# Kernel tuning notes

Measured on AMD Instinct MI355X. Metric: run time of the kernel, lower is better.

The kernel has to match this reference:

```python
import jax, jax.numpy as jnp
import numpy as np

N_SUPPORT = 131072
NUM_CLASSES = 1024
D = 512
NUM_LEVELS = 3
LN_EPS = 1e-5


def setup_inputs() -> dict:
    key = jax.random.key(0)
    ks = jax.random.split(key, 10)
    s = 1.0 / np.sqrt(D)
    return {
        "support_features": jax.random.normal(ks[0], (N_SUPPORT, D), dtype=jnp.float32),
        "support_labels": jax.random.randint(ks[1], (N_SUPPORT,), 0, NUM_CLASSES, dtype=jnp.int32),
        "W1": jax.random.normal(ks[2], (NUM_LEVELS, D, D), dtype=jnp.float32) * s,
        "b1": jnp.zeros((NUM_LEVELS, D), dtype=jnp.float32),
        "ln_gamma": jnp.ones((NUM_LEVELS, D), dtype=jnp.float32),
        "ln_beta": jnp.zeros((NUM_LEVELS, D), dtype=jnp.float32),
        "W2": jax.random.normal(ks[3], (NUM_LEVELS, D, D), dtype=jnp.float32) * s,
        "b2": jnp.zeros((NUM_LEVELS, D), dtype=jnp.float32),
        "level_temperatures": jnp.ones((NUM_LEVELS,), dtype=jnp.float32),
    }


def _prototype_level(x, labels, w1, bb1, gamma, beta, w2, bb2, counts):
    # MLP: Linear -> LayerNorm -> ReLU -> (Dropout=identity, eval) -> Linear
    h = x @ w1 + bb1                                   # [N, D]
    mu = jnp.mean(h, axis=-1, keepdims=True)
    var = jnp.mean(jnp.square(h - mu), axis=-1, keepdims=True)
    h = (h - mu) * jax.lax.rsqrt(var + LN_EPS) * gamma + beta
    h = jax.nn.relu(h)
    h = h @ w2 + bb2                                   # [N, D]
    # per-class mean prototype (segment mean)
    sums = jax.ops.segment_sum(h, labels, num_segments=NUM_CLASSES)  # [C, D]
    return sums / counts


def reference(support_features, support_labels, W1, b1, ln_gamma, ln_beta, W2, b2, level_temperatures):
    labels = support_labels.astype(jnp.int32)
    counts = jax.ops.segment_sum(
        jnp.ones((support_features.shape[0],), dtype=support_features.dtype),
        labels, num_segments=NUM_CLASSES)
    counts = jnp.maximum(counts, 1.0)[:, None]         # [C, 1]

    level_protos = jax.vmap(
        lambda w1, bb1, g, bt, w2, bb2: _prototype_level(
            support_features, labels, w1, bb1, g, bt, w2, bb2, counts)
    )(W1, b1, ln_gamma, ln_beta, W2, b2)               # [L, C, D]

    level_weights = jax.nn.softmax(level_temperatures)  # [L]
    final_prototypes = jnp.einsum('l,lcd->cd', level_weights, level_protos)
    return final_prototypes
```

## Files before the change

### kernel.cpp

```cpp
#include <hip/hip_runtime.h>
#include <hip/hip_bf16.h>
#include <cstdint>

#define N_SUPPORT 131072
#define NUM_CLASSES 1024
#define DIM 512
#define LN_EPS 1e-5f

typedef __attribute__((ext_vector_type(8))) short bf16x8;
typedef __attribute__((ext_vector_type(4))) float f32x4;

__device__ __forceinline__ unsigned short f2bf(float f) {
  union { float f; uint32_t u; } c; c.f = f;
  uint32_t u = c.u;
  u += 0x7fffu + ((u >> 16) & 1u);
  return (unsigned short)(u >> 16);
}
__device__ __forceinline__ float bf2f(unsigned short h) {
  union { uint32_t u; float f; } c; c.u = ((uint32_t)h) << 16;
  return c.f;
}

__device__ __forceinline__ void gload16(const void* g, void* l) {
  __builtin_amdgcn_global_load_lds((const __attribute__((address_space(1))) void*)g,
                                   (__attribute__((address_space(3))) void*)l,
                                   16, 0, 0);
}

__global__ void k_cast_x(const float* __restrict__ x, unsigned short* __restrict__ xb) {
  const size_t i = ((size_t)blockIdx.x * blockDim.x + threadIdx.x) * 8;
  float4 a = *(const float4*)(x + i);
  float4 b = *(const float4*)(x + i + 4);
  uint4 o;
  o.x = (uint32_t)f2bf(a.x) | ((uint32_t)f2bf(a.y) << 16);
  o.y = (uint32_t)f2bf(a.z) | ((uint32_t)f2bf(a.w) << 16);
  o.z = (uint32_t)f2bf(b.x) | ((uint32_t)f2bf(b.y) << 16);
  o.w = (uint32_t)f2bf(b.z) | ((uint32_t)f2bf(b.w) << 16);
  *(uint4*)(xb + i) = o;
}

__global__ void k_prep_w1t(const float* __restrict__ w1, unsigned short* __restrict__ w1t) {
  const int idx = blockIdx.x * 256 + threadIdx.x;
  const int l = idx >> 18;
  const int rem = idx & 262143;
  const int k = rem >> 9;
  const int n = rem & 511;
  w1t[((size_t)l * 512 + n) * 512 + k] = f2bf(w1[idx]);
}

__global__ void k_hist(const int* __restrict__ labels, int* __restrict__ counts) {
  const int i = blockIdx.x * 256 + threadIdx.x;
  atomicAdd(&counts[labels[i]], 1);
}

__global__ void k_scan(const int* __restrict__ counts, int* __restrict__ offs) {
  __shared__ int tmp[1024];
  const int t = threadIdx.x;
  const int myc = counts[t];
  tmp[t] = myc;
  __syncthreads();
  for (int o = 1; o < 1024; o <<= 1) {
    int v = (t >= o) ? tmp[t - o] : 0;
    __syncthreads();
    tmp[t] += v;
    __syncthreads();
  }
  offs[t] = tmp[t] - myc;
}

__global__ void k_scatter(const int* __restrict__ labels, const int* __restrict__ offs,
                          int* __restrict__ cursor, int* __restrict__ sorted) {
  const int i = blockIdx.x * 256 + threadIdx.x;
  const int c = labels[i];
  const int p = atomicAdd(&cursor[c], 1);
  sorted[offs[c] + p] = i;
}

__global__ __launch_bounds__(256, 2) void k_gemm1ln(
    const unsigned short* __restrict__ Xb, const unsigned short* __restrict__ W1T,
    const float* __restrict__ b1, const float* __restrict__ gamma, const float* __restrict__ beta,
    unsigned short* __restrict__ g, int l)
{
  __shared__ unsigned short sX[64 * 32];
  __shared__ unsigned short sW[512 * 32];
  __shared__ float wsum[4][64];
  __shared__ float wsq[4][64];
  __shared__ float smean[64];
  __shared__ float srstd[64];

  const int t = threadIdx.x;
  const int wv = t >> 6;
  const int lane = t & 63;
  const int lr = lane & 15;
  const int lq = lane >> 4;
  const int row0 = blockIdx.x * 64;

  const unsigned short* Wl = W1T + (size_t)l * 512 * 512;

  f32x4 acc[4][8];
  #pragma unroll
  for (int i = 0; i < 4; ++i)
    #pragma unroll
    for (int j = 0; j < 8; ++j) acc[i][j] = (f32x4){0.f, 0.f, 0.f, 0.f};

  const int xrow = t >> 2;
  const int ko8 = (t & 3) * 8;
  const unsigned short* xg = Xb + (size_t)(row0 + xrow) * 512 + ko8;
  unsigned short* sXw = sX + wv * 512;

  for (int ks = 0; ks < 16; ++ks) {
    const int kk = ks * 32;
    gload16(xg + kk, sXw);
    #pragma unroll
    for (int i = 0; i < 8; ++i) {
      const int n = i * 64 + (t >> 2);
      gload16(Wl + (size_t)n * 512 + kk + ko8, sW + (i * 256 + wv * 64) * 8);
    }
    __syncthreads();

    bf16x8 a[4], b[8];
    #pragma unroll
    for (int rf = 0; rf < 4; ++rf)
      a[rf] = *(const bf16x8*)(sX + (rf * 16 + lr) * 32 + lq * 8);
    #pragma unroll
    for (int cf = 0; cf < 8; ++cf)
      b[cf] = *(const bf16x8*)(sW + (wv * 128 + cf * 16 + lr) * 32 + lq * 8);

    #pragma unroll
    for (int rf = 0; rf < 4; ++rf)
      #pragma unroll
      for (int cf = 0; cf < 8; ++cf)
        acc[rf][cf] = __builtin_amdgcn_mfma_f32_16x16x32_bf16(a[rf], b[cf], acc[rf][cf], 0, 0, 0);
    __syncthreads();
  }

  float b1v[8], gv[8], bv[8];
  #pragma unroll
  for (int cf = 0; cf < 8; ++cf) {
    const int col = wv * 128 + cf * 16 + lr;
    b1v[cf] = b1[l * 512 + col];
    gv[cf] = gamma[l * 512 + col];
    bv[cf] = beta[l * 512 + col];
  }
  #pragma unroll
  for (int rf = 0; rf < 4; ++rf)
    #pragma unroll
    for (int cf = 0; cf < 8; ++cf)
      #pragma unroll
      for (int j = 0; j < 4; ++j) acc[rf][cf][j] += b1v[cf];

  #pragma unroll
  for (int rf = 0; rf < 4; ++rf) {
    #pragma unroll
    for (int j = 0; j < 4; ++j) {
      float s = 0.f, q = 0.f;
      #pragma unroll
      for (int cf = 0; cf < 8; ++cf) { float v = acc[rf][cf][j]; s += v; q += v * v; }
      #pragma unroll
      for (int m = 8; m >= 1; m >>= 1) { s += __shfl_xor(s, m, 16); q += __shfl_xor(q, m, 16); }
      if (lr == 0) { const int row = rf * 16 + lq * 4 + j; wsum[wv][row] = s; wsq[wv][row] = q; }
    }
  }
  __syncthreads();
  if (t < 64) {
    const float s = wsum[0][t] + wsum[1][t] + wsum[2][t] + wsum[3][t];
    const float q = wsq[0][t] + wsq[1][t] + wsq[2][t] + wsq[3][t];
    const float mean = s * (1.0f / 512.0f);
    const float var = q * (1.0f / 512.0f) - mean * mean;
    smean[t] = mean;
    srstd[t] = rsqrtf(var + LN_EPS);
  }
  __syncthreads();

  #pragma unroll
  for (int rf = 0; rf < 4; ++rf) {
    #pragma unroll
    for (int j = 0; j < 4; ++j) {
      const int row = rf * 16 + lq * 4 + j;
      const float mean = smean[row], rs = srstd[row];
      unsigned short* go = g + (size_t)(row0 + row) * 512 + wv * 128 + lr;
      #pragma unroll
      for (int cf = 0; cf < 8; ++cf) {
        float v = (acc[rf][cf][j] - mean) * rs * gv[cf] + bv[cf];
        v = fmaxf(v, 0.f);
        go[cf * 16] = f2bf(v);
      }
    }
  }
}

__global__ void k_reduce(const unsigned short* __restrict__ g, const int* __restrict__ sorted,
                         const int* __restrict__ offs, const int* __restrict__ counts,
                         float* __restrict__ M, int l)
{
  __shared__ int sidx[256];
  const int c = blockIdx.x;
  const int t = threadIdx.x;
  const int beg = offs[c];
  const int n = counts[c];
  float a0 = 0.f, a1 = 0.f;
  for (int base = 0; base < n; base += 256) {
    const int m = min(256, n - base);
    __syncthreads();
    if (t < m) sidx[t] = sorted[beg + base + t];
    __syncthreads();
    for (int r = 0; r < m; ++r) {
      const uint32_t v = *(const uint32_t*)(g + (size_t)sidx[r] * 512 + t * 2);
      a0 += bf2f((unsigned short)(v & 0xffffu));
      a1 += bf2f((unsigned short)(v >> 16));
    }
  }
  const float inv = 1.0f / (float)max(n, 1);
  float* out = M + ((size_t)l * 1024 + c) * 512 + t * 2;
  out[0] = a0 * inv;
  out[1] = a1 * inv;
}

__global__ void k_final(const float* __restrict__ M, const float* __restrict__ W2,
                        const float* __restrict__ b2, const float* __restrict__ temps,
                        float* __restrict__ out)
{
  __shared__ float sA[64][17];
  __shared__ float sB[16][65];
  const int t = threadIdx.x;
  const int tx = t & 15, ty = t >> 4;
  const int bcol = blockIdx.x * 64;
  const int brow = blockIdx.y * 64;

  const float t0 = temps[0], t1 = temps[1], t2 = temps[2];
  const float mx = fmaxf(t0, fmaxf(t1, t2));
  const float e0 = expf(t0 - mx), e1 = expf(t1 - mx), e2 = expf(t2 - mx);
  const float inv = 1.f / (e0 + e1 + e2);
  const float w[3] = {e0 * inv, e1 * inv, e2 * inv};

  float acc[4][4] = {};
  for (int l = 0; l < 3; ++l) {
    for (int k0 = 0; k0 < 512; k0 += 16) {
      __syncthreads();
      #pragma unroll
      for (int i = 0; i < 4; ++i) {
        const int e = i * 256 + t;
        const int r = e >> 4, k = e & 15;
        sA[r][k] = M[((size_t)l * 1024 + brow + r) * 512 + k0 + k] * w[l];
      }
      #pragma unroll
      for (int i = 0; i < 4; ++i) {
        const int e = i * 256 + t;
        const int r = e >> 6, nn = e & 63;
        sB[r][nn] = W2[((size_t)l * 512 + k0 + r) * 512 + bcol + nn];
      }
      __syncthreads();
      #pragma unroll
      for (int kk = 0; kk < 16; ++kk) {
        float a[4], b[4];
        #pragma unroll
        for (int i = 0; i < 4; ++i) a[i] = sA[ty * 4 + i][kk];
        #pragma unroll
        for (int j = 0; j < 4; ++j) b[j] = sB[kk][tx * 4 + j];
        #pragma unroll
        for (int i = 0; i < 4; ++i)
          #pragma unroll
          for (int j = 0; j < 4; ++j) acc[i][j] += a[i] * b[j];
      }
    }
  }
  #pragma unroll
  for (int j = 0; j < 4; ++j) {
    const int col = bcol + tx * 4 + j;
    const float bias = w[0] * b2[col] + w[1] * b2[512 + col] + w[2] * b2[1024 + col];
    #pragma unroll
    for (int i = 0; i < 4; ++i)
      out[(size_t)(brow + ty * 4 + i) * 512 + col] = acc[i][j] + bias;
  }
}

extern "C" void kernel_launch(void* const* d_in, const int* in_sizes, int n_in,
                              void* d_out, int out_size, void* d_ws, size_t ws_size,
                              hipStream_t stream)
{
  const float* X = (const float*)d_in[0];
  const int* labels = (const int*)d_in[1];
  const float* W1 = (const float*)d_in[2];
  const float* b1 = (const float*)d_in[3];
  const float* gamma = (const float*)d_in[4];
  const float* beta = (const float*)d_in[5];
  const float* W2 = (const float*)d_in[6];
  const float* b2 = (const float*)d_in[7];
  const float* temps = (const float*)d_in[8];
  float* out = (float*)d_out;

  char* ws = (char*)d_ws;
  size_t off = 0;
  auto alloc = [&](size_t bytes) -> char* {
    char* p = ws + off;
    off += (bytes + 255) & ~(size_t)255;
    return p;
  };
  unsigned short* Xb = (unsigned short*)alloc((size_t)N_SUPPORT * DIM * 2);
  unsigned short* gbuf = (unsigned short*)alloc((size_t)N_SUPPORT * DIM * 2);
  unsigned short* W1T = (unsigned short*)alloc((size_t)3 * 512 * 512 * 2);
  float* M = (float*)alloc((size_t)3 * 1024 * 512 * 4);
  int* counts = (int*)alloc(2048 * 4);
  int* cursor = counts + 1024;
  int* offs = (int*)alloc(1024 * 4);
  int* sorted = (int*)alloc((size_t)N_SUPPORT * 4);
  (void)cursor;

  hipMemsetAsync(counts, 0, 2048 * 4, stream);
  k_cast_x<<<32768, 256, 0, stream>>>(X, Xb);
  k_prep_w1t<<<3072, 256, 0, stream>>>(W1, W1T);
  k_hist<<<512, 256, 0, stream>>>(labels, counts);
  k_scan<<<1, 1024, 0, stream>>>(counts, offs);
  k_scatter<<<512, 256, 0, stream>>>(labels, offs, cursor, sorted);
  for (int l = 0; l < 3; ++l) {
    k_gemm1ln<<<2048, 256, 0, stream>>>(Xb, W1T, b1, gamma, beta, gbuf, l);
    k_reduce<<<1024, 256, 0, stream>>>(gbuf, sorted, offs, counts, M, l);
  }
  k_final<<<dim3(8, 16), 256, 0, stream>>>(M, W2, b2, temps, out);
}
```

Baseline: 1.026 ms.

## Sort rows by class and fuse segment reduction into GEMM1+LayerNorm epilogue

Rows of X are gathered into class-sorted order during the bf16 cast, so each 64-row GEMM tile covers only a few contiguous class runs. The GEMM1+LayerNorm+ReLU kernel then sums each run in registers with shuffles and atomically adds the result into the per-class accumulator M. This drops the 128 MB bf16 intermediate write and the separate gather-reduce kernel for each level. The division by class count moves into the final kernel through a precomputed inverse-count array. In exchange it adds a serial run scan per tile, global float atomics, an extra memset of M, and order-dependent float summation.

```diff
diff --git a/kernel.cpp b/kernel.cpp
--- a/kernel.cpp
+++ b/kernel.cpp
@@ -16,10 +16,6 @@
   u += 0x7fffu + ((u >> 16) & 1u);
   return (unsigned short)(u >> 16);
 }
-__device__ __forceinline__ float bf2f(unsigned short h) {
-  union { uint32_t u; float f; } c; c.u = ((uint32_t)h) << 16;
-  return c.f;
-}
 
 __device__ __forceinline__ void gload16(const void* g, void* l) {
   __builtin_amdgcn_global_load_lds((const __attribute__((address_space(1))) void*)g,
@@ -27,33 +23,13 @@
                                    16, 0, 0);
 }
 
-__global__ void k_cast_x(const float* __restrict__ x, unsigned short* __restrict__ xb) {
-  const size_t i = ((size_t)blockIdx.x * blockDim.x + threadIdx.x) * 8;
-  float4 a = *(const float4*)(x + i);
-  float4 b = *(const float4*)(x + i + 4);
-  uint4 o;
-  o.x = (uint32_t)f2bf(a.x) | ((uint32_t)f2bf(a.y) << 16);
-  o.y = (uint32_t)f2bf(a.z) | ((uint32_t)f2bf(a.w) << 16);
-  o.z = (uint32_t)f2bf(b.x) | ((uint32_t)f2bf(b.y) << 16);
-  o.w = (uint32_t)f2bf(b.z) | ((uint32_t)f2bf(b.w) << 16);
-  *(uint4*)(xb + i) = o;
-}
-
-__global__ void k_prep_w1t(const float* __restrict__ w1, unsigned short* __restrict__ w1t) {
-  const int idx = blockIdx.x * 256 + threadIdx.x;
-  const int l = idx >> 18;
-  const int rem = idx & 262143;
-  const int k = rem >> 9;
-  const int n = rem & 511;
-  w1t[((size_t)l * 512 + n) * 512 + k] = f2bf(w1[idx]);
-}
-
 __global__ void k_hist(const int* __restrict__ labels, int* __restrict__ counts) {
   const int i = blockIdx.x * 256 + threadIdx.x;
   atomicAdd(&counts[labels[i]], 1);
 }
 
-__global__ void k_scan(const int* __restrict__ counts, int* __restrict__ offs) {
+__global__ void k_scan(const int* __restrict__ counts, int* __restrict__ offs,
+                       float* __restrict__ invc) {
   __shared__ int tmp[1024];
   const int t = threadIdx.x;
   const int myc = counts[t];
@@ -66,6 +42,7 @@
     __syncthreads();
   }
   offs[t] = tmp[t] - myc;
+  invc[t] = 1.0f / (float)max(myc, 1);
 }
 
 __global__ void k_scatter(const int* __restrict__ labels, const int* __restrict__ offs,
@@ -76,10 +53,37 @@
   sorted[offs[c] + p] = i;
 }
 
-__global__ __launch_bounds__(256, 2) void k_gemm1ln(
+__global__ void k_cast_sorted(const float* __restrict__ x, const int* __restrict__ sorted,
+                              const int* __restrict__ labels,
+                              unsigned short* __restrict__ xb, int* __restrict__ scls) {
+  const int p = blockIdx.x * 4 + (threadIdx.x >> 6);
+  const int src = sorted[p];
+  const int k = (threadIdx.x & 63) * 8;
+  const float* xr = x + (size_t)src * DIM + k;
+  float4 a = *(const float4*)(xr);
+  float4 b = *(const float4*)(xr + 4);
+  uint4 o;
+  o.x = (uint32_t)f2bf(a.x) | ((uint32_t)f2bf(a.y) << 16);
+  o.y = (uint32_t)f2bf(a.z) | ((uint32_t)f2bf(a.w) << 16);
+  o.z = (uint32_t)f2bf(b.x) | ((uint32_t)f2bf(b.y) << 16);
+  o.w = (uint32_t)f2bf(b.z) | ((uint32_t)f2bf(b.w) << 16);
+  *(uint4*)(xb + (size_t)p * DIM + k) = o;
+  if ((threadIdx.x & 63) == 0) scls[p] = labels[src];
+}
+
+__global__ void k_prep_w1t(const float* __restrict__ w1, unsigned short* __restrict__ w1t) {
+  const int idx = blockIdx.x * 256 + threadIdx.x;
+  const int l = idx >> 18;
+  const int rem = idx & 262143;
+  const int k = rem >> 9;
+  const int n = rem & 511;
+  w1t[((size_t)l * 512 + n) * 512 + k] = f2bf(w1[idx]);
+}
+
+__global__ __launch_bounds__(256, 2) void k_gemm1lnred(
     const unsigned short* __restrict__ Xb, const unsigned short* __restrict__ W1T,
     const float* __restrict__ b1, const float* __restrict__ gamma, const float* __restrict__ beta,
-    unsigned short* __restrict__ g, int l)
+    const int* __restrict__ scls_g, float* __restrict__ M, int l)
 {
   __shared__ unsigned short sX[64 * 32];
   __shared__ unsigned short sW[512 * 32];
@@ -87,6 +91,10 @@
   __shared__ float wsq[4][64];
   __shared__ float smean[64];
   __shared__ float srstd[64];
+  __shared__ int scls[64];
+  __shared__ int run_start[65];
+  __shared__ int run_cls[64];
+  __shared__ int nruns_s;
 
   const int t = threadIdx.x;
   const int wv = t >> 6;
@@ -107,6 +115,8 @@
   const int ko8 = (t & 3) * 8;
   const unsigned short* xg = Xb + (size_t)(row0 + xrow) * 512 + ko8;
   unsigned short* sXw = sX + wv * 512;
+
+  if (t < 64) scls[t] = scls_g[row0 + t];
 
   for (int ks = 0; ks < 16; ++ks) {
     const int kk = ks * 32;
@@ -170,6 +180,16 @@
     smean[t] = mean;
     srstd[t] = rsqrtf(var + LN_EPS);
   }
+  if (t == 0) {
+    int n = 0;
+    run_start[0] = 0;
+    run_cls[0] = scls[0];
+    for (int r = 1; r < 64; ++r) {
+      if (scls[r] != scls[r - 1]) { ++n; run_start[n] = r; run_cls[n] = scls[r]; }
+    }
+    nruns_s = n + 1;
+    run_start[n + 1] = 64;
+  }
   __syncthreads();
 
   #pragma unroll
@@ -178,47 +198,49 @@
     for (int j = 0; j < 4; ++j) {
       const int row = rf * 16 + lq * 4 + j;
       const float mean = smean[row], rs = srstd[row];
-      unsigned short* go = g + (size_t)(row0 + row) * 512 + wv * 128 + lr;
       #pragma unroll
       for (int cf = 0; cf < 8; ++cf) {
         float v = (acc[rf][cf][j] - mean) * rs * gv[cf] + bv[cf];
-        v = fmaxf(v, 0.f);
-        go[cf * 16] = f2bf(v);
-      }
-    }
-  }
-}
-
-__global__ void k_reduce(const unsigned short* __restrict__ g, const int* __restrict__ sorted,
-                         const int* __restrict__ offs, const int* __restrict__ counts,
-                         float* __restrict__ M, int l)
-{
-  __shared__ int sidx[256];
-  const int c = blockIdx.x;
-  const int t = threadIdx.x;
-  const int beg = offs[c];
-  const int n = counts[c];
-  float a0 = 0.f, a1 = 0.f;
-  for (int base = 0; base < n; base += 256) {
-    const int m = min(256, n - base);
-    __syncthreads();
-    if (t < m) sidx[t] = sorted[beg + base + t];
-    __syncthreads();
-    for (int r = 0; r < m; ++r) {
-      const uint32_t v = *(const uint32_t*)(g + (size_t)sidx[r] * 512 + t * 2);
-      a0 += bf2f((unsigned short)(v & 0xffffu));
-      a1 += bf2f((unsigned short)(v >> 16));
-    }
-  }
-  const float inv = 1.0f / (float)max(n, 1);
-  float* out = M + ((size_t)l * 1024 + c) * 512 + t * 2;
-  out[0] = a0 * inv;
-  out[1] = a1 * inv;
+        acc[rf][cf][j] = fmaxf(v, 0.f);
+      }
+    }
+  }
+
+  const int nruns = nruns_s;
+  float* Ml = M + (size_t)l * NUM_CLASSES * DIM;
+  for (int r = 0; r < nruns; ++r) {
+    const int rs = run_start[r], re = run_start[r + 1];
+    const int cls = run_cls[r];
+    float p[8];
+    #pragma unroll
+    for (int cf = 0; cf < 8; ++cf) p[cf] = 0.f;
+    #pragma unroll
+    for (int rf = 0; rf < 4; ++rf) {
+      #pragma unroll
+      for (int j = 0; j < 4; ++j) {
+        const int row = rf * 16 + lq * 4 + j;
+        if (row >= rs && row < re) {
+          #pragma unroll
+          for (int cf = 0; cf < 8; ++cf) p[cf] += acc[rf][cf][j];
+        }
+      }
+    }
+    #pragma unroll
+    for (int cf = 0; cf < 8; ++cf) {
+      p[cf] += __shfl_xor(p[cf], 16);
+      p[cf] += __shfl_xor(p[cf], 32);
+    }
+    if (lq == 0) {
+      #pragma unroll
+      for (int cf = 0; cf < 8; ++cf)
+        atomicAdd(&Ml[(size_t)cls * DIM + wv * 128 + cf * 16 + lr], p[cf]);
+    }
+  }
 }
 
 __global__ void k_final(const float* __restrict__ M, const float* __restrict__ W2,
                         const float* __restrict__ b2, const float* __restrict__ temps,
-                        float* __restrict__ out)
+                        const float* __restrict__ invc, float* __restrict__ out)
 {
   __shared__ float sA[64][17];
   __shared__ float sB[16][65];
@@ -241,7 +263,7 @@
       for (int i = 0; i < 4; ++i) {
         const int e = i * 256 + t;
         const int r = e >> 4, k = e & 15;
-        sA[r][k] = M[((size_t)l * 1024 + brow + r) * 512 + k0 + k] * w[l];
+        sA[r][k] = M[((size_t)l * 1024 + brow + r) * 512 + k0 + k] * (w[l] * invc[brow + r]);
       }
       #pragma unroll
       for (int i = 0; i < 4; ++i) {
@@ -297,24 +319,24 @@
     return p;
   };
   unsigned short* Xb = (unsigned short*)alloc((size_t)N_SUPPORT * DIM * 2);
-  unsigned short* gbuf = (unsigned short*)alloc((size_t)N_SUPPORT * DIM * 2);
   unsigned short* W1T = (unsigned short*)alloc((size_t)3 * 512 * 512 * 2);
   float* M = (float*)alloc((size_t)3 * 1024 * 512 * 4);
   int* counts = (int*)alloc(2048 * 4);
   int* cursor = counts + 1024;
   int* offs = (int*)alloc(1024 * 4);
+  float* invc = (float*)alloc(1024 * 4);
   int* sorted = (int*)alloc((size_t)N_SUPPORT * 4);
-  (void)cursor;
+  int* scls = (int*)alloc((size_t)N_SUPPORT * 4);
 
   hipMemsetAsync(counts, 0, 2048 * 4, stream);
-  k_cast_x<<<32768, 256, 0, stream>>>(X, Xb);
+  hipMemsetAsync(M, 0, (size_t)3 * 1024 * 512 * 4, stream);
+  k_hist<<<512, 256, 0, stream>>>(labels, counts);
+  k_scan<<<1, 1024, 0, stream>>>(counts, offs, invc);
+  k_scatter<<<512, 256, 0, stream>>>(labels, offs, cursor, sorted);
+  k_cast_sorted<<<32768, 256, 0, stream>>>(X, sorted, labels, Xb, scls);
   k_prep_w1t<<<3072, 256, 0, stream>>>(W1, W1T);
-  k_hist<<<512, 256, 0, stream>>>(labels, counts);
-  k_scan<<<1, 1024, 0, stream>>>(counts, offs);
-  k_scatter<<<512, 256, 0, stream>>>(labels, offs, cursor, sorted);
   for (int l = 0; l < 3; ++l) {
-    k_gemm1ln<<<2048, 256, 0, stream>>>(Xb, W1T, b1, gamma, beta, gbuf, l);
-    k_reduce<<<1024, 256, 0, stream>>>(gbuf, sorted, offs, counts, M, l);
-  }
-  k_final<<<dim3(8, 16), 256, 0, stream>>>(M, W2, b2, temps, out);
-}
+    k_gemm1lnred<<<2048, 256, 0, stream>>>(Xb, W1T, b1, gamma, beta, scls, M, l);
+  }
+  k_final<<<dim3(8, 16), 256, 0, stream>>>(M, W2, b2, temps, invc, out);
+}
```

After: 954.3 us. -7.0%, faster.
